# Optimization experiments

Measured on AMD Instinct MI355X. Metric: run time of the kernel, lower is better.

## Reference

```python
import jax, jax.numpy as jnp
import numpy as np

# Module hyperparameters (match torch init_kwargs)
D_MODEL = 512
N_HEADS = 8
WINDOW_LEN = 128
DIL_FACTOR = 64
N_DIL = 2
ATTN_SINK = True
SRC_LEN = 2048
BSZ = 2


def setup_inputs() -> dict:
    key = jax.random.key(0)
    ks = jax.random.split(key, 6)
    w_scale = 0.04  # ~ xavier_uniform scale for 512x512
    inp = {
        "x": jax.random.normal(ks[0], (SRC_LEN, BSZ, D_MODEL), jnp.float32),
        "Wq": jax.random.normal(ks[1], (D_MODEL, D_MODEL), jnp.float32) * w_scale,
        "bq": jnp.zeros((D_MODEL,), jnp.float32),
        "Wk": jax.random.normal(ks[2], (D_MODEL, D_MODEL), jnp.float32) * w_scale,
        "bk": jnp.zeros((D_MODEL,), jnp.float32),
        "Wv": jax.random.normal(ks[3], (D_MODEL, D_MODEL), jnp.float32) * w_scale,
        "bv": jnp.zeros((D_MODEL,), jnp.float32),
        "Wo": jax.random.normal(ks[4], (D_MODEL, D_MODEL), jnp.float32) * w_scale,
        "bo": jnp.zeros((D_MODEL,), jnp.float32),
        "beta": jnp.zeros((N_HEADS,), jnp.float32),
    }
    return inp


def _fast_attention(x, Wq, bq, Wk, bk, Wv, bv, Wo, bo, beta):
    s, b, dm = x.shape  # (src_len, bsz, d_model)
    h = N_HEADS
    d = dm // h
    q = x @ Wq.T + bq
    k = x @ Wk.T + bk
    v = x @ Wv.T + bv

    def split_heads(t):  # 's b (h d) -> (b h) s d'
        return t.reshape(s, b, h, d).transpose(1, 2, 0, 3).reshape(b * h, s, d)

    q, k, v = split_heads(q), split_heads(k), split_heads(v)

    # beta: per-head temperature, tiled over batch (matches torch .repeat(bsz,1,1))
    beta_e = jnp.tile(jnp.exp(beta), b)[:, None, None]  # (b*h, 1, 1)
    q = q / (jnp.sqrt(jnp.asarray(d, q.dtype)) * beta_e)

    attn_out = jnp.zeros_like(v)
    z = b * h
    for i in range(N_DIL):
        dil = DIL_FACTOR ** i
        p = (WINDOW_LEN - 1) * dil
        pad = (p % s) if (p % s) != p else 0  # static python ints
        nw = pad // dil + 1  # num windows
        # causal left-padded strided windowed view of q: (z, nw, s, d)
        qp = jnp.pad(q, ((0, 0), (pad, 0), (0, 0)))
        idx = (jnp.arange(nw) * dil)[:, None] + jnp.arange(s)[None, :]  # (nw, s)
        qi = qp[:, idx, :]
        w = jnp.einsum('zbsd,zsd->zbs', qi, k)  # (z, nw, s)
        if ATTN_SINK:
            w = jnp.concatenate([w, jnp.zeros((z, 1, s), w.dtype)], axis=1)
        w = jax.nn.softmax(w, axis=1)  # softmax over window axis (+ sink)
        if ATTN_SINK:
            w = w[:, :-1]
        k2 = jnp.einsum('zbs,zsd->zbd', w, k)  # (z, nw, d)
        v2 = jnp.einsum('zbs,zsd->zbd', w, v)
        # left-pad back to full length (zeros at front, values at end)
        k = jnp.pad(k2, ((0, 0), (s - nw, 0), (0, 0)))
        v = jnp.pad(v2, ((0, 0), (s - nw, 0), (0, 0)))
        attn_out = attn_out + v

    # '(b h) s d -> s b (h d)'
    out = attn_out.reshape(b, h, s, d).transpose(2, 0, 1, 3).reshape(s, b, dm)
    return out @ Wo.T + bo


def reference(x, Wq, bq, Wk, bk, Wv, bv, Wo, bo, beta):
    return _fast_attention(x, Wq, bq, Wk, bk, Wv, bv, Wo, bo, beta)
```

## Files before the change

### kernel.cpp

```cpp
#include <hip/hip_runtime.h>
#include <hip/hip_bf16.h>
#include <math.h>

#define S_LEN 2048
#define BSZ 2
#define DM 512
#define NH 8
#define HD 64
#define RTOT (S_LEN*BSZ)
#define T_KEEP 32
#define ROW0 ((S_LEN - T_KEEP)*BSZ)
#define NXELEM (RTOT*DM)
#define NWROW  (NH*128)
#define NWELEM (NWROW*DM)

typedef __attribute__((ext_vector_type(8))) _Float16 half8;
typedef __attribute__((ext_vector_type(4))) float floatx4;

__device__ __forceinline__ void gld16(const void* g, void* l) {
    __builtin_amdgcn_global_load_lds((const __attribute__((address_space(1))) void*)g,
                                     (__attribute__((address_space(3))) void*)l, 16, 0, 0);
}

__device__ __forceinline__ short cvt1(float v) {
    _Float16 h = (_Float16)v;
    return __builtin_bit_cast(short, h);
}

__global__ __launch_bounds__(256) void convert(
    const float* __restrict__ x,
    const float* __restrict__ Wq, const float* __restrict__ Wk,
    const float* __restrict__ bq, const float* __restrict__ bk,
    const float* __restrict__ bo,
    short* __restrict__ xf, short* __restrict__ wf, float* __restrict__ bcat,
    float* __restrict__ sig, float* __restrict__ sbar, float* __restrict__ Ssum,
    float* __restrict__ out)
{
    const int g = blockIdx.x*blockDim.x + threadIdx.x;
    const int stride = gridDim.x*blockDim.x;
    const int total4 = (NXELEM + NWELEM)/4;
    for (int i = g; i < total4; i += stride) {
        float4 v; size_t dst; short* d;
        if (i < NXELEM/4) {
            v = ((const float4*)x)[i];
            dst = (size_t)i*4; d = xf;
        } else {
            int e = (i - NXELEM/4)*4;
            int R = e >> 9;
            int k = e & 511;
            int h = R >> 7;
            int p = R & 127;
            int m = p >> 6;
            int c = p & 63;
            const float* W = m ? Wk : Wq;
            v = *(const float4*)&W[(size_t)(h*HD + c)*DM + k];
            dst = (size_t)R*DM + k; d = wf;
        }
        short4 hv;
        hv.x = cvt1(v.x); hv.y = cvt1(v.y); hv.z = cvt1(v.z); hv.w = cvt1(v.w);
        *(short4*)&d[dst] = hv;
    }
    {
        const float4* b4 = (const float4*)bo;
        float4* o4 = (float4*)out;
        const int fill4 = ROW0*DM/4;
        for (int i = g; i < fill4; i += stride) o4[i] = b4[i & 127];
    }
    if (g < NWROW) {
        int h = g >> 7, p = g & 127, m = p >> 6, c = p & 63;
        bcat[g] = (m ? bk : bq)[h*HD + c];
    }
    if (g < NH*RTOT) sig[g] = 0.f;
    if (g < 16*DM)   sbar[g] = 0.f;
    if (g < 16)      Ssum[g] = 0.f;
}

__global__ __launch_bounds__(256, 2) void qk_gemm(
    const _Float16* __restrict__ xf, const _Float16* __restrict__ wf,
    const float* __restrict__ bcat,
    float* __restrict__ sig, float* __restrict__ qsel)
{
    __shared__ __align__(16) char smem[65536];

    const int tid  = threadIdx.x;
    const int w    = tid >> 6;
    const int lane = tid & 63;
    const int lrow = lane & 15;
    const int lk8  = lane >> 4;
    const int rc   = blockIdx.x;
    const int h    = blockIdx.y;
    const int jh   = blockIdx.z;
    const int r0   = rc * 128;

    {
        const int t = w;
        const int bcol = (t < 2) ? (jh*32 + t*16) : (64 + jh*32 + (t-2)*16);
        const _Float16* src = wf + (size_t)(h*128 + bcol + lrow)*DM + lk8*8;
        for (int ci = 0; ci < 16; ++ci)
            gld16(src + ci*32, smem + (w*16 + ci)*1024);
    }
    __syncthreads();

    const float bq0 = bcat[h*128 + jh*32 + lrow];
    const float bq1 = bcat[h*128 + jh*32 + 16 + lrow];
    const float bk0 = bcat[h*128 + 64 + jh*32 + lrow];
    const float bk1 = bcat[h*128 + 64 + jh*32 + 16 + lrow];

    #pragma unroll
    for (int nn = 0; nn < 2; ++nn) {
        const int n = w + nn*4;
        const int rbase = r0 + n*16;

        half8 A[16];
        const _Float16* pa = xf + (size_t)(rbase + lrow)*DM + lk8*8;
        #pragma unroll
        for (int kc = 0; kc < 16; ++kc)
            A[kc] = *(const half8*)(pa + kc*32);

        floatx4 aq0 = (floatx4)0.f, aq1 = (floatx4)0.f;
        floatx4 ak0 = (floatx4)0.f, ak1 = (floatx4)0.f;
        #pragma unroll
        for (int kc = 0; kc < 16; ++kc) {
            half8 b0 = *(const half8*)(smem + ( 0 + kc)*1024 + lane*16);
            half8 b1 = *(const half8*)(smem + (16 + kc)*1024 + lane*16);
            half8 b2 = *(const half8*)(smem + (32 + kc)*1024 + lane*16);
            half8 b3 = *(const half8*)(smem + (48 + kc)*1024 + lane*16);
            aq0 = __builtin_amdgcn_mfma_f32_16x16x32_f16(A[kc], b0, aq0, 0, 0, 0);
            aq1 = __builtin_amdgcn_mfma_f32_16x16x32_f16(A[kc], b1, aq1, 0, 0, 0);
            ak0 = __builtin_amdgcn_mfma_f32_16x16x32_f16(A[kc], b2, ak0, 0, 0, 0);
            ak1 = __builtin_amdgcn_mfma_f32_16x16x32_f16(A[kc], b3, ak1, 0, 0, 0);
        }

        #pragma unroll
        for (int r = 0; r < 4; ++r) {
            float q0 = aq0[r] + bq0, q1 = aq1[r] + bq1;
            float k0 = ak0[r] + bk0, k1 = ak1[r] + bk1;
            float p = q0*k0 + q1*k1;
            p += __shfl_xor(p, 1, 64);
            p += __shfl_xor(p, 2, 64);
            p += __shfl_xor(p, 4, 64);
            p += __shfl_xor(p, 8, 64);
            int row = rbase + lk8*4 + r;
            if (lrow == 0) atomicAdd(&sig[h*RTOT + row], p);
            if (((row >> 1) & 63) == 63) {
                int b  = row & 1;
                int wi = row >> 7;
                float* qd = &qsel[((size_t)(b*NH + h)*T_KEEP + wi)*64];
                qd[jh*32 + lrow]      = q0;
                qd[jh*32 + 16 + lrow] = q1;
            }
        }
    }
}

__global__ __launch_bounds__(256) void sbark(
    const float* __restrict__ x, const float* __restrict__ sigr,
    const float* __restrict__ beta, float* __restrict__ sbar,
    float* __restrict__ Ssum)
{
    __shared__ float ss[64][NH];
    const int tid = threadIdx.x;
    const int b = blockIdx.x & 1;
    const int s0 = (blockIdx.x >> 1) * 64;

    for (int i = tid; i < 64*NH; i += 256) {
        int s = i >> 3, hh = i & 7;
        float raw = sigr[hh*RTOT + (s0 + s)*2 + b];
        float isc = 1.0f / (8.0f * expf(beta[hh]));
        ss[s][hh] = 1.0f / (1.0f + expf(-raw * isc));
    }
    __syncthreads();
    if (tid < NH) {
        float t = 0.f;
        for (int s = 0; s < 64; ++s) t += ss[s][tid];
        atomicAdd(&Ssum[b*NH + tid], t);
    }
    #pragma unroll
    for (int cp = 0; cp < 2; ++cp) {
        int c = cp*256 + tid;
        float a8[NH];
        #pragma unroll
        for (int hh = 0; hh < NH; ++hh) a8[hh] = 0.f;
        for (int s = 0; s < 64; ++s) {
            float xv = x[(size_t)((s0 + s)*2 + b)*DM + c];
            #pragma unroll
            for (int hh = 0; hh < NH; ++hh) a8[hh] += ss[s][hh] * xv;
        }
        #pragma unroll
        for (int hh = 0; hh < NH; ++hh)
            atomicAdd(&sbar[(b*NH + hh)*DM + c], a8[hh]);
    }
}

__global__ __launch_bounds__(256) void headk(
    const float* __restrict__ qsel, const float* __restrict__ beta,
    const float* __restrict__ sbar, const float* __restrict__ Ssum,
    const float* __restrict__ Wk, const float* __restrict__ bk,
    const float* __restrict__ Wv, const float* __restrict__ bv,
    const float* __restrict__ Wo,
    float* __restrict__ coef, float* __restrict__ G)
{
    const int z = blockIdx.x;
    const int h = z & 7;
    const int tid = threadIdx.x;

    __shared__ float s_sb[DM];
    __shared__ float s_red[64][4];
    __shared__ float s_kb[64], s_vb[64];
    __shared__ float s_part[T_KEEP][8];
    __shared__ float s_gp[64][4];

    s_sb[tid]       = sbar[z*DM + tid];
    s_sb[tid + 256] = sbar[z*DM + 256 + tid];
    __syncthreads();
    const float S = Ssum[z];

    {
        int j = tid >> 2, kp = tid & 3;
        const float* wr = &Wk[(size_t)(h*HD + j)*DM + kp*128];
        float a = 0.f;
        #pragma unroll
        for (int k = 0; k < 128; k += 4) {
            float4 w4 = *(const float4*)&wr[k];
            int k0 = kp*128 + k;
            a += w4.x*s_sb[k0] + w4.y*s_sb[k0+1] + w4.z*s_sb[k0+2] + w4.w*s_sb[k0+3];
        }
        s_red[j][kp] = a;
    }
    __syncthreads();
    if (tid < 64) s_kb[tid] = s_red[tid][0]+s_red[tid][1]+s_red[tid][2]+s_red[tid][3]
                              + bk[h*HD + tid]*S;
    __syncthreads();
    {
        int j = tid >> 2, kp = tid & 3;
        const float* wr = &Wv[(size_t)(h*HD + j)*DM + kp*128];
        float a = 0.f;
        #pragma unroll
        for (int k = 0; k < 128; k += 4) {
            float4 w4 = *(const float4*)&wr[k];
            int k0 = kp*128 + k;
            a += w4.x*s_sb[k0] + w4.y*s_sb[k0+1] + w4.z*s_sb[k0+2] + w4.w*s_sb[k0+3];
        }
        s_red[j][kp] = a;
    }
    __syncthreads();
    if (tid < 64) s_vb[tid] = s_red[tid][0]+s_red[tid][1]+s_red[tid][2]+s_red[tid][3]
                              + bv[h*HD + tid]*S;
    __syncthreads();

    {
        int wi = tid >> 3, jg = tid & 7;
        const float* qrow = &qsel[((size_t)z*T_KEEP + wi)*64 + jg*8];
        float4 q1 = *(const float4*)qrow;
        float4 q2 = *(const float4*)(qrow + 4);
        int j0 = jg*8;
        float p = q1.x*s_kb[j0] + q1.y*s_kb[j0+1] + q1.z*s_kb[j0+2] + q1.w*s_kb[j0+3]
                + q2.x*s_kb[j0+4] + q2.y*s_kb[j0+5] + q2.z*s_kb[j0+6] + q2.w*s_kb[j0+7];
        s_part[wi][jg] = p;
    }
    __syncthreads();
    if (tid < T_KEEP) {
        float sc = 0.f;
        #pragma unroll
        for (int gg = 0; gg < 8; ++gg) sc += s_part[tid][gg];
        sc *= 1.0f / (8.0f * expf(beta[h]));
        float m = sc;
        #pragma unroll
        for (int off = 16; off > 0; off >>= 1) m = fmaxf(m, __shfl_xor(m, off, 64));
        m = fmaxf(m, 0.f);
        float e = expf(sc - m);
        float d = e;
        #pragma unroll
        for (int off = 16; off > 0; off >>= 1) d += __shfl_xor(d, off, 64);
        d += expf(-m);
        float c = e / d;
        if (tid == T_KEEP-1) c += 1.0f;
        coef[z*T_KEEP + tid] = c;
    }

    const int cq = tid >> 2;
    const int jg = tid & 3;
    #pragma unroll
    for (int it = 0; it < 8; ++it) {
        int c = it*64 + cq;
        const float* wrow = &Wo[(size_t)c*DM + h*HD + jg*16];
        float a = 0.f;
        #pragma unroll
        for (int jj = 0; jj < 16; jj += 4) {
            float4 wv = *(const float4*)&wrow[jj];
            int j0 = jg*16 + jj;
            a += wv.x*s_vb[j0] + wv.y*s_vb[j0+1] + wv.z*s_vb[j0+2] + wv.w*s_vb[j0+3];
        }
        s_gp[cq][jg] = a;
        __syncthreads();
        if (tid < 64)
            G[(size_t)z*DM + it*64 + tid] = s_gp[tid][0] + s_gp[tid][1] + s_gp[tid][2] + s_gp[tid][3];
        __syncthreads();
    }
}

__global__ __launch_bounds__(256) void outk3(
    const float* __restrict__ coef, const float* __restrict__ G,
    const float* __restrict__ bo, float* __restrict__ out)
{
    const int a = blockIdx.x;
    const int b = a & 1;
    const int wi = a >> 1;
    const int tid = threadIdx.x;
    __shared__ float s_cf[NH];
    if (tid < NH) s_cf[tid] = coef[(b*NH + tid)*T_KEEP + wi];
    __syncthreads();
    for (int c = tid; c < DM; c += 256) {
        float v = bo[c];
        #pragma unroll
        for (int h = 0; h < NH; ++h)
            v += s_cf[h] * G[(size_t)(b*NH + h)*DM + c];
        out[(size_t)(ROW0 + a)*DM + c] = v;
    }
}

extern "C" void kernel_launch(void* const* d_in, const int* in_sizes, int n_in,
                              void* d_out, int out_size, void* d_ws, size_t ws_size,
                              hipStream_t stream) {
    const float* x    = (const float*)d_in[0];
    const float* Wq   = (const float*)d_in[1];
    const float* bq   = (const float*)d_in[2];
    const float* Wk   = (const float*)d_in[3];
    const float* bk   = (const float*)d_in[4];
    const float* Wv   = (const float*)d_in[5];
    const float* bv   = (const float*)d_in[6];
    const float* Wo   = (const float*)d_in[7];
    const float* bo   = (const float*)d_in[8];
    const float* beta = (const float*)d_in[9];

    char* ws = (char*)d_ws;
    float* sig  = (float*)(ws + 0);
    float* qsel = (float*)(ws + 131072);
    float* sbar = (float*)(ws + 262144);
    float* Ssum = (float*)(ws + 294912);
    float* bcat = (float*)(ws + 295168);
    float* coef = (float*)(ws + 299264);
    float* G    = (float*)(ws + 301312);
    short* xf   = (short*)(ws + 335872);
    short* wf   = (short*)(ws + 335872 + 4194304);
    float* out  = (float*)d_out;

    convert<<<2048, 256, 0, stream>>>(x, Wq, Wk, bq, bk, bo,
                                      xf, wf, bcat, sig, sbar, Ssum, out);
    dim3 g1(32, NH, 2);
    qk_gemm<<<g1, 256, 0, stream>>>((const _Float16*)xf, (const _Float16*)wf,
                                    bcat, sig, qsel);
    sbark<<<64, 256, 0, stream>>>(x, sig, beta, sbar, Ssum);
    headk<<<16, 256, 0, stream>>>(qsel, beta, sbar, Ssum, Wk, bk, Wv, bv, Wo, coef, G);
    outk3<<<64, 256, 0, stream>>>(coef, G, bo, out);
}
```

Measured before the change: 125.6 us.

## Pre-swizzle fp16 operands into MFMA fragment layout and remove atomics

```diff
diff --git a/kernel.cpp b/kernel.cpp
--- a/kernel.cpp
+++ b/kernel.cpp
@@ -1,5 +1,4 @@
 #include <hip/hip_runtime.h>
-#include <hip/hip_bf16.h>
 #include <math.h>
 
 #define S_LEN 2048
@@ -10,9 +9,6 @@
 #define RTOT (S_LEN*BSZ)
 #define T_KEEP 32
 #define ROW0 ((S_LEN - T_KEEP)*BSZ)
-#define NXELEM (RTOT*DM)
-#define NWROW  (NH*128)
-#define NWELEM (NWROW*DM)
 
 typedef __attribute__((ext_vector_type(8))) _Float16 half8;
 typedef __attribute__((ext_vector_type(4))) float floatx4;
@@ -27,57 +23,57 @@
     return __builtin_bit_cast(short, h);
 }
 
-__global__ __launch_bounds__(256) void convert(
-    const float* __restrict__ x,
-    const float* __restrict__ Wq, const float* __restrict__ Wk,
-    const float* __restrict__ bq, const float* __restrict__ bk,
-    const float* __restrict__ bo,
-    short* __restrict__ xf, short* __restrict__ wf, float* __restrict__ bcat,
-    float* __restrict__ sig, float* __restrict__ sbar, float* __restrict__ Ssum,
-    float* __restrict__ out)
-{
-    const int g = blockIdx.x*blockDim.x + threadIdx.x;
-    const int stride = gridDim.x*blockDim.x;
-    const int total4 = (NXELEM + NWELEM)/4;
-    for (int i = g; i < total4; i += stride) {
-        float4 v; size_t dst; short* d;
-        if (i < NXELEM/4) {
-            v = ((const float4*)x)[i];
-            dst = (size_t)i*4; d = xf;
-        } else {
-            int e = (i - NXELEM/4)*4;
-            int R = e >> 9;
-            int k = e & 511;
-            int h = R >> 7;
-            int p = R & 127;
-            int m = p >> 6;
-            int c = p & 63;
-            const float* W = m ? Wk : Wq;
-            v = *(const float4*)&W[(size_t)(h*HD + c)*DM + k];
-            dst = (size_t)R*DM + k; d = wf;
-        }
-        short4 hv;
-        hv.x = cvt1(v.x); hv.y = cvt1(v.y); hv.z = cvt1(v.z); hv.w = cvt1(v.w);
-        *(short4*)&d[dst] = hv;
-    }
-    {
+__global__ __launch_bounds__(256) void convert2(
+    const float* __restrict__ x, const float* __restrict__ Wq,
+    const float* __restrict__ Wk, const float* __restrict__ bo,
+    short* __restrict__ xfrag, short* __restrict__ wfrag, float* __restrict__ out)
+{
+    __shared__ short sm[8192];
+    const int bx = blockIdx.x;
+    const int tid = threadIdx.x;
+    if (bx >= 320) {
+        int g = (bx - 320)*256 + tid;
         const float4* b4 = (const float4*)bo;
         float4* o4 = (float4*)out;
         const int fill4 = ROW0*DM/4;
-        for (int i = g; i < fill4; i += stride) o4[i] = b4[i & 127];
-    }
-    if (g < NWROW) {
-        int h = g >> 7, p = g & 127, m = p >> 6, c = p & 63;
-        bcat[g] = (m ? bk : bq)[h*HD + c];
-    }
-    if (g < NH*RTOT) sig[g] = 0.f;
-    if (g < 16*DM)   sbar[g] = 0.f;
-    if (g < 16)      Ssum[g] = 0.f;
+        for (int i = g; i < fill4; i += 512*256) o4[i] = b4[i & 127];
+        return;
+    }
+    const float* src;
+    short* dst;
+    if (bx < 256) {
+        src = x + (size_t)bx*16*DM;
+        dst = xfrag + (size_t)bx*16*DM;
+    } else {
+        int wt = bx - 256;
+        int h = wt >> 3, jh = (wt >> 2) & 1, t = wt & 3;
+        int m = t >> 1, sub = t & 1;
+        const float* W = m ? Wk : Wq;
+        src = W + (size_t)(h*HD + jh*32 + sub*16)*DM;
+        dst = wfrag + (size_t)((h*2 + jh)*64 + t*16)*512;
+    }
+    #pragma unroll
+    for (int it = 0; it < 8; ++it) {
+        int f4 = it*256 + tid;
+        int row = f4 >> 7, k4 = f4 & 127;
+        float4 v = ((const float4*)src)[row*128 + k4];
+        short4 hv;
+        hv.x = cvt1(v.x); hv.y = cvt1(v.y); hv.z = cvt1(v.z); hv.w = cvt1(v.w);
+        int kc = k4 >> 3, lk8 = (k4 >> 1) & 3, ho = (k4 & 1)*4;
+        *(short4*)&sm[(kc*64 + lk8*16 + row)*8 + ho] = hv;
+    }
+    __syncthreads();
+    #pragma unroll
+    for (int it = 0; it < 4; ++it) {
+        int p = it*256 + tid;
+        uint4 v = *(const uint4*)&sm[p*8];
+        *(uint4*)&dst[p*8] = v;
+    }
 }
 
 __global__ __launch_bounds__(256, 2) void qk_gemm(
-    const _Float16* __restrict__ xf, const _Float16* __restrict__ wf,
-    const float* __restrict__ bcat,
+    const short* __restrict__ xfrag, const short* __restrict__ wfrag,
+    const float* __restrict__ bq, const float* __restrict__ bk,
     float* __restrict__ sig, float* __restrict__ qsel)
 {
     __shared__ __align__(16) char smem[65536];
@@ -90,32 +86,29 @@
     const int rc   = blockIdx.x;
     const int h    = blockIdx.y;
     const int jh   = blockIdx.z;
-    const int r0   = rc * 128;
-
-    {
-        const int t = w;
-        const int bcol = (t < 2) ? (jh*32 + t*16) : (64 + jh*32 + (t-2)*16);
-        const _Float16* src = wf + (size_t)(h*128 + bcol + lrow)*DM + lk8*8;
+
+    {
+        const short* src = wfrag + ((size_t)(h*2 + jh)*64 + w*16)*512 + lane*8;
         for (int ci = 0; ci < 16; ++ci)
-            gld16(src + ci*32, smem + (w*16 + ci)*1024);
-    }
-    __syncthreads();
-
-    const float bq0 = bcat[h*128 + jh*32 + lrow];
-    const float bq1 = bcat[h*128 + jh*32 + 16 + lrow];
-    const float bk0 = bcat[h*128 + 64 + jh*32 + lrow];
-    const float bk1 = bcat[h*128 + 64 + jh*32 + 16 + lrow];
+            gld16(src + ci*512, smem + (w*16 + ci)*1024);
+    }
+    __syncthreads();
+
+    const float bq0 = bq[h*HD + jh*32 + lrow];
+    const float bq1 = bq[h*HD + jh*32 + 16 + lrow];
+    const float bk0 = bk[h*HD + jh*32 + lrow];
+    const float bk1 = bk[h*HD + jh*32 + 16 + lrow];
 
     #pragma unroll
     for (int nn = 0; nn < 2; ++nn) {
-        const int n = w + nn*4;
-        const int rbase = r0 + n*16;
+        const int rt = rc*8 + w + nn*4;
+        const int rbase = rt*16;
 
         half8 A[16];
-        const _Float16* pa = xf + (size_t)(rbase + lrow)*DM + lk8*8;
+        const short* pa = xfrag + (size_t)rt*8192 + lane*8;
         #pragma unroll
         for (int kc = 0; kc < 16; ++kc)
-            A[kc] = *(const half8*)(pa + kc*32);
+            A[kc] = *(const half8*)(pa + kc*512);
 
         floatx4 aq0 = (floatx4)0.f, aq1 = (floatx4)0.f;
         floatx4 ak0 = (floatx4)0.f, ak1 = (floatx4)0.f;
@@ -141,7 +134,7 @@
             p += __shfl_xor(p, 4, 64);
             p += __shfl_xor(p, 8, 64);
             int row = rbase + lk8*4 + r;
-            if (lrow == 0) atomicAdd(&sig[h*RTOT + row], p);
+            if (lrow == 0) sig[((size_t)jh*NH + h)*RTOT + row] = p;
             if (((row >> 1) & 63) == 63) {
                 int b  = row & 1;
                 int wi = row >> 7;
@@ -154,41 +147,64 @@
 }
 
 __global__ __launch_bounds__(256) void sbark(
-    const float* __restrict__ x, const float* __restrict__ sigr,
+    const float* __restrict__ x, const float* __restrict__ sig,
     const float* __restrict__ beta, float* __restrict__ sbar,
     float* __restrict__ Ssum)
 {
-    __shared__ float ss[64][NH];
+    __shared__ float ss[256*8];
+    __shared__ float s_red[2048];
     const int tid = threadIdx.x;
     const int b = blockIdx.x & 1;
-    const int s0 = (blockIdx.x >> 1) * 64;
-
-    for (int i = tid; i < 64*NH; i += 256) {
-        int s = i >> 3, hh = i & 7;
-        float raw = sigr[hh*RTOT + (s0 + s)*2 + b];
-        float isc = 1.0f / (8.0f * expf(beta[hh]));
-        ss[s][hh] = 1.0f / (1.0f + expf(-raw * isc));
-    }
-    __syncthreads();
-    if (tid < NH) {
-        float t = 0.f;
-        for (int s = 0; s < 64; ++s) t += ss[s][tid];
-        atomicAdd(&Ssum[b*NH + tid], t);
-    }
-    #pragma unroll
-    for (int cp = 0; cp < 2; ++cp) {
-        int c = cp*256 + tid;
-        float a8[NH];
-        #pragma unroll
-        for (int hh = 0; hh < NH; ++hh) a8[hh] = 0.f;
-        for (int s = 0; s < 64; ++s) {
-            float xv = x[(size_t)((s0 + s)*2 + b)*DM + c];
+    const int cc = (blockIdx.x >> 1)*32;
+    const int col = tid & 31, sgrp = tid >> 5;
+    const int hld = tid & 7, sld = tid >> 3;
+    const float is = 1.0f / (8.0f * expf(beta[hld]));
+
+    float a8[8];
+    #pragma unroll
+    for (int hh = 0; hh < 8; ++hh) a8[hh] = 0.f;
+    float tsum = 0.f;
+
+    for (int scn = 0; scn < 8; ++scn) {
+        const int s0 = scn*256;
+        #pragma unroll
+        for (int j = 0; j < 8; ++j) {
+            int sl = sld + 32*j;
+            int s = s0 + sl;
+            float raw = sig[(size_t)hld*RTOT + s*2 + b]
+                      + sig[(size_t)(NH + hld)*RTOT + s*2 + b];
+            float sv = 1.0f / (1.0f + expf(-raw * is));
+            ss[sl*8 + hld] = sv;
+            tsum += sv;
+        }
+        __syncthreads();
+        for (int j = 0; j < 32; ++j) {
+            int sl = sgrp + j*8;
+            float xv = x[(size_t)((s0 + sl)*2 + b)*DM + cc + col];
             #pragma unroll
-            for (int hh = 0; hh < NH; ++hh) a8[hh] += ss[s][hh] * xv;
-        }
-        #pragma unroll
-        for (int hh = 0; hh < NH; ++hh)
-            atomicAdd(&sbar[(b*NH + hh)*DM + c], a8[hh]);
+            for (int hh = 0; hh < 8; ++hh) a8[hh] += ss[sl*8 + hh] * xv;
+        }
+        __syncthreads();
+    }
+    #pragma unroll
+    for (int hh = 0; hh < 8; ++hh) s_red[(sgrp*32 + col)*8 + hh] = a8[hh];
+    __syncthreads();
+    {
+        int hh = tid >> 5, c2 = tid & 31;
+        float a = 0.f;
+        #pragma unroll
+        for (int sg = 0; sg < 8; ++sg) a += s_red[(sg*32 + c2)*8 + hh];
+        sbar[(size_t)(b*NH + hh)*DM + cc + c2] = a;
+    }
+    if (cc == 0) {
+        __syncthreads();
+        s_red[tid] = tsum;
+        __syncthreads();
+        if (tid < 8) {
+            float t = 0.f;
+            for (int i = tid; i < 256; i += 8) t += s_red[i];
+            Ssum[b*NH + tid] = t;
+        }
     }
 }
 
@@ -334,23 +350,20 @@
     const float* beta = (const float*)d_in[9];
 
     char* ws = (char*)d_ws;
-    float* sig  = (float*)(ws + 0);
-    float* qsel = (float*)(ws + 131072);
-    float* sbar = (float*)(ws + 262144);
-    float* Ssum = (float*)(ws + 294912);
-    float* bcat = (float*)(ws + 295168);
-    float* coef = (float*)(ws + 299264);
-    float* G    = (float*)(ws + 301312);
-    short* xf   = (short*)(ws + 335872);
-    short* wf   = (short*)(ws + 335872 + 4194304);
-    float* out  = (float*)d_out;
-
-    convert<<<2048, 256, 0, stream>>>(x, Wq, Wk, bq, bk, bo,
-                                      xf, wf, bcat, sig, sbar, Ssum, out);
+    float* sig   = (float*)(ws + 0);
+    float* qsel  = (float*)(ws + 262144);
+    float* sbar  = (float*)(ws + 393216);
+    float* Ssum  = (float*)(ws + 425984);
+    float* coef  = (float*)(ws + 426240);
+    float* G     = (float*)(ws + 428288);
+    short* xfrag = (short*)(ws + 461056);
+    short* wfrag = (short*)(ws + 461056 + 4194304);
+    float* out   = (float*)d_out;
+
+    convert2<<<832, 256, 0, stream>>>(x, Wq, Wk, bo, xfrag, wfrag, out);
     dim3 g1(32, NH, 2);
-    qk_gemm<<<g1, 256, 0, stream>>>((const _Float16*)xf, (const _Float16*)wf,
-                                    bcat, sig, qsel);
-    sbark<<<64, 256, 0, stream>>>(x, sig, beta, sbar, Ssum);
+    qk_gemm<<<g1, 256, 0, stream>>>(xfrag, wfrag, bq, bk, sig, qsel);
+    sbark<<<32, 256, 0, stream>>>(x, sig, beta, sbar, Ssum);
     headk<<<16, 256, 0, stream>>>(qsel, beta, sbar, Ssum, Wk, bk, Wv, bv, Wo, coef, G);
     outk3<<<64, 256, 0, stream>>>(coef, G, bo, out);
 }
```

Result: slower. 142.2 us (+13.2%).

## Fuse five kernels into one persistent kernel with grid barriers

Applied to the files above, without the earlier changes.

```diff
diff --git a/kernel.cpp b/kernel.cpp
--- a/kernel.cpp
+++ b/kernel.cpp
@@ -1,5 +1,4 @@
 #include <hip/hip_runtime.h>
-#include <hip/hip_bf16.h>
 #include <math.h>
 
 #define S_LEN 2048
@@ -13,6 +12,8 @@
 #define NXELEM (RTOT*DM)
 #define NWROW  (NH*128)
 #define NWELEM (NWROW*DM)
+#define GRID   512
+#define NTHR   (GRID*256)
 
 typedef __attribute__((ext_vector_type(8))) _Float16 half8;
 typedef __attribute__((ext_vector_type(4))) float floatx4;
@@ -27,295 +28,301 @@
     return __builtin_bit_cast(short, h);
 }
 
-__global__ __launch_bounds__(256) void convert(
+__device__ __forceinline__ void gridbar(unsigned* cnt, int idx) {
+    __syncthreads();
+    __threadfence();
+    if (threadIdx.x == 0) {
+        atomicAdd(&cnt[idx], 1u);
+        unsigned it = 0;
+        while (atomicAdd(&cnt[idx], 0u) < (unsigned)GRID && it < 2000000u) {
+            __builtin_amdgcn_s_sleep(8);
+            ++it;
+        }
+    }
+    __syncthreads();
+    __threadfence();
+}
+
+__global__ __launch_bounds__(256, 2) void fused(
     const float* __restrict__ x,
-    const float* __restrict__ Wq, const float* __restrict__ Wk,
-    const float* __restrict__ bq, const float* __restrict__ bk,
-    const float* __restrict__ bo,
+    const float* __restrict__ Wq, const float* __restrict__ bq,
+    const float* __restrict__ Wk, const float* __restrict__ bk,
+    const float* __restrict__ Wv, const float* __restrict__ bv,
+    const float* __restrict__ Wo, const float* __restrict__ bo,
+    const float* __restrict__ beta,
     short* __restrict__ xf, short* __restrict__ wf, float* __restrict__ bcat,
-    float* __restrict__ sig, float* __restrict__ sbar, float* __restrict__ Ssum,
-    float* __restrict__ out)
-{
-    const int g = blockIdx.x*blockDim.x + threadIdx.x;
-    const int stride = gridDim.x*blockDim.x;
-    const int total4 = (NXELEM + NWELEM)/4;
-    for (int i = g; i < total4; i += stride) {
-        float4 v; size_t dst; short* d;
-        if (i < NXELEM/4) {
-            v = ((const float4*)x)[i];
-            dst = (size_t)i*4; d = xf;
-        } else {
-            int e = (i - NXELEM/4)*4;
-            int R = e >> 9;
-            int k = e & 511;
-            int h = R >> 7;
-            int p = R & 127;
-            int m = p >> 6;
-            int c = p & 63;
-            const float* W = m ? Wk : Wq;
-            v = *(const float4*)&W[(size_t)(h*HD + c)*DM + k];
-            dst = (size_t)R*DM + k; d = wf;
-        }
-        short4 hv;
-        hv.x = cvt1(v.x); hv.y = cvt1(v.y); hv.z = cvt1(v.z); hv.w = cvt1(v.w);
-        *(short4*)&d[dst] = hv;
-    }
-    {
-        const float4* b4 = (const float4*)bo;
-        float4* o4 = (float4*)out;
-        const int fill4 = ROW0*DM/4;
-        for (int i = g; i < fill4; i += stride) o4[i] = b4[i & 127];
-    }
-    if (g < NWROW) {
-        int h = g >> 7, p = g & 127, m = p >> 6, c = p & 63;
-        bcat[g] = (m ? bk : bq)[h*HD + c];
-    }
-    if (g < NH*RTOT) sig[g] = 0.f;
-    if (g < 16*DM)   sbar[g] = 0.f;
-    if (g < 16)      Ssum[g] = 0.f;
-}
-
-__global__ __launch_bounds__(256, 2) void qk_gemm(
-    const _Float16* __restrict__ xf, const _Float16* __restrict__ wf,
-    const float* __restrict__ bcat,
-    float* __restrict__ sig, float* __restrict__ qsel)
+    float* __restrict__ sig, float* __restrict__ qsel,
+    float* __restrict__ sbar, float* __restrict__ Ssum,
+    float* __restrict__ coef, float* __restrict__ G,
+    unsigned* __restrict__ cnt, float* __restrict__ out)
 {
     __shared__ __align__(16) char smem[65536];
-
-    const int tid  = threadIdx.x;
-    const int w    = tid >> 6;
-    const int lane = tid & 63;
-    const int lrow = lane & 15;
-    const int lk8  = lane >> 4;
-    const int rc   = blockIdx.x;
-    const int h    = blockIdx.y;
-    const int jh   = blockIdx.z;
-    const int r0   = rc * 128;
+    const int bid = blockIdx.x;
+    const int tid = threadIdx.x;
 
     {
-        const int t = w;
-        const int bcol = (t < 2) ? (jh*32 + t*16) : (64 + jh*32 + (t-2)*16);
-        const _Float16* src = wf + (size_t)(h*128 + bcol + lrow)*DM + lk8*8;
-        for (int ci = 0; ci < 16; ++ci)
-            gld16(src + ci*32, smem + (w*16 + ci)*1024);
-    }
-    __syncthreads();
-
-    const float bq0 = bcat[h*128 + jh*32 + lrow];
-    const float bq1 = bcat[h*128 + jh*32 + 16 + lrow];
-    const float bk0 = bcat[h*128 + 64 + jh*32 + lrow];
-    const float bk1 = bcat[h*128 + 64 + jh*32 + 16 + lrow];
-
-    #pragma unroll
-    for (int nn = 0; nn < 2; ++nn) {
-        const int n = w + nn*4;
-        const int rbase = r0 + n*16;
-
-        half8 A[16];
-        const _Float16* pa = xf + (size_t)(rbase + lrow)*DM + lk8*8;
+        const int g = bid*256 + tid;
+        const int total4 = (NXELEM + NWELEM)/4;
+        for (int i = g; i < total4; i += NTHR) {
+            float4 v; size_t dst; short* d;
+            if (i < NXELEM/4) {
+                v = ((const float4*)x)[i];
+                dst = (size_t)i*4; d = xf;
+            } else {
+                int e = (i - NXELEM/4)*4;
+                int R = e >> 9;
+                int k = e & 511;
+                int h = R >> 7;
+                int p = R & 127;
+                int m = p >> 6;
+                int c = p & 63;
+                const float* W = m ? Wk : Wq;
+                v = *(const float4*)&W[(size_t)(h*HD + c)*DM + k];
+                dst = (size_t)R*DM + k; d = wf;
+            }
+            short4 hv;
+            hv.x = cvt1(v.x); hv.y = cvt1(v.y); hv.z = cvt1(v.z); hv.w = cvt1(v.w);
+            *(short4*)&d[dst] = hv;
+        }
+        {
+            const float4* b4 = (const float4*)bo;
+            float4* o4 = (float4*)out;
+            const int fill4 = ROW0*DM/4;
+            for (int i = g; i < fill4; i += NTHR) o4[i] = b4[i & 127];
+        }
+        if (g < NWROW) {
+            int h = g >> 7, p = g & 127, m = p >> 6, c = p & 63;
+            bcat[g] = (m ? bk : bq)[h*HD + c];
+        }
+        if (g < NH*RTOT) sig[g] = 0.f;
+        if (g < 16*DM)   sbar[g] = 0.f;
+        if (g < 16)      Ssum[g] = 0.f;
+    }
+    gridbar(cnt, 0);
+
+    {
+        const int w    = tid >> 6;
+        const int lane = tid & 63;
+        const int lrow = lane & 15;
+        const int lk8  = lane >> 4;
+        const int rc   = bid & 31;
+        const int h    = (bid >> 5) & 7;
+        const int jh   = bid >> 8;
+        const int r0   = rc * 128;
+
+        {
+            const int t = w;
+            const int bcol = (t < 2) ? (jh*32 + t*16) : (64 + jh*32 + (t-2)*16);
+            const short* src = wf + (size_t)(h*128 + bcol + lrow)*DM + lk8*8;
+            for (int ci = 0; ci < 16; ++ci)
+                gld16(src + ci*32, smem + (w*16 + ci)*1024);
+        }
+        __syncthreads();
+
+        const float bq0 = bcat[h*128 + jh*32 + lrow];
+        const float bq1 = bcat[h*128 + jh*32 + 16 + lrow];
+        const float bk0 = bcat[h*128 + 64 + jh*32 + lrow];
+        const float bk1 = bcat[h*128 + 64 + jh*32 + 16 + lrow];
+
         #pragma unroll
-        for (int kc = 0; kc < 16; ++kc)
-            A[kc] = *(const half8*)(pa + kc*32);
-
-        floatx4 aq0 = (floatx4)0.f, aq1 = (floatx4)0.f;
-        floatx4 ak0 = (floatx4)0.f, ak1 = (floatx4)0.f;
+        for (int nn = 0; nn < 2; ++nn) {
+            const int n = w + nn*4;
+            const int rbase = r0 + n*16;
+
+            half8 A[16];
+            const short* pa = xf + (size_t)(rbase + lrow)*DM + lk8*8;
+            #pragma unroll
+            for (int kc = 0; kc < 16; ++kc)
+                A[kc] = *(const half8*)(pa + kc*32);
+
+            floatx4 aq0 = (floatx4)0.f, aq1 = (floatx4)0.f;
+            floatx4 ak0 = (floatx4)0.f, ak1 = (floatx4)0.f;
+            #pragma unroll
+            for (int kc = 0; kc < 16; ++kc) {
+                half8 b0 = *(const half8*)(smem + ( 0 + kc)*1024 + lane*16);
+                half8 b1 = *(const half8*)(smem + (16 + kc)*1024 + lane*16);
+                half8 b2 = *(const half8*)(smem + (32 + kc)*1024 + lane*16);
+                half8 b3 = *(const half8*)(smem + (48 + kc)*1024 + lane*16);
+                aq0 = __builtin_amdgcn_mfma_f32_16x16x32_f16(A[kc], b0, aq0, 0, 0, 0);
+                aq1 = __builtin_amdgcn_mfma_f32_16x16x32_f16(A[kc], b1, aq1, 0, 0, 0);
+                ak0 = __builtin_amdgcn_mfma_f32_16x16x32_f16(A[kc], b2, ak0, 0, 0, 0);
+                ak1 = __builtin_amdgcn_mfma_f32_16x16x32_f16(A[kc], b3, ak1, 0, 0, 0);
+            }
+
+            #pragma unroll
+            for (int r = 0; r < 4; ++r) {
+                float q0 = aq0[r] + bq0, q1 = aq1[r] + bq1;
+                float k0 = ak0[r] + bk0, k1 = ak1[r] + bk1;
+                float p = q0*k0 + q1*k1;
+                p += __shfl_xor(p, 1, 64);
+                p += __shfl_xor(p, 2, 64);
+                p += __shfl_xor(p, 4, 64);
+                p += __shfl_xor(p, 8, 64);
+                int row = rbase + lk8*4 + r;
+                if (lrow == 0) atomicAdd(&sig[h*RTOT + row], p);
+                if (((row >> 1) & 63) == 63) {
+                    int b  = row & 1;
+                    int wi = row >> 7;
+                    float* qd = &qsel[((size_t)(b*NH + h)*T_KEEP + wi)*64];
+                    qd[jh*32 + lrow]      = q0;
+                    qd[jh*32 + 16 + lrow] = q1;
+                }
+            }
+        }
+    }
+    gridbar(cnt, 1);
+
+    if (bid < 64) {
+        float* ss = (float*)smem;
+        const int b = bid & 1;
+        const int s0 = (bid >> 1) * 64;
+
+        for (int i = tid; i < 64*NH; i += 256) {
+            int s = i >> 3, hh = i & 7;
+            float raw = sig[hh*RTOT + (s0 + s)*2 + b];
+            float isc = 1.0f / (8.0f * expf(beta[hh]));
+            ss[s*8 + hh] = 1.0f / (1.0f + expf(-raw * isc));
+        }
+        __syncthreads();
+        if (tid < NH) {
+            float t = 0.f;
+            for (int s = 0; s < 64; ++s) t += ss[s*8 + tid];
+            atomicAdd(&Ssum[b*NH + tid], t);
+        }
         #pragma unroll
-        for (int kc = 0; kc < 16; ++kc) {
-            half8 b0 = *(const half8*)(smem + ( 0 + kc)*1024 + lane*16);
-            half8 b1 = *(const half8*)(smem + (16 + kc)*1024 + lane*16);
-            half8 b2 = *(const half8*)(smem + (32 + kc)*1024 + lane*16);
-            half8 b3 = *(const half8*)(smem + (48 + kc)*1024 + lane*16);
-            aq0 = __builtin_amdgcn_mfma_f32_16x16x32_f16(A[kc], b0, aq0, 0, 0, 0);
-            aq1 = __builtin_amdgcn_mfma_f32_16x16x32_f16(A[kc], b1, aq1, 0, 0, 0);
-            ak0 = __builtin_amdgcn_mfma_f32_16x16x32_f16(A[kc], b2, ak0, 0, 0, 0);
-            ak1 = __builtin_amdgcn_mfma_f32_16x16x32_f16(A[kc], b3, ak1, 0, 0, 0);
-        }
-
+        for (int cp = 0; cp < 2; ++cp) {
+            int c = cp*256 + tid;
+            float a8[NH];
+            #pragma unroll
+            for (int hh = 0; hh < NH; ++hh) a8[hh] = 0.f;
+            for (int s = 0; s < 64; ++s) {
+                float xv = x[(size_t)((s0 + s)*2 + b)*DM + c];
+                #pragma unroll
+                for (int hh = 0; hh < NH; ++hh) a8[hh] += ss[s*8 + hh] * xv;
+            }
+            #pragma unroll
+            for (int hh = 0; hh < NH; ++hh)
+                atomicAdd(&sbar[(b*NH + hh)*DM + c], a8[hh]);
+        }
+    }
+    gridbar(cnt, 2);
+
+    if (bid < 16) {
+        float* F = (float*)smem;
+        float* s_sb   = F;
+        float* s_red  = F + 512;
+        float* s_kb   = F + 768;
+        float* s_vb   = F + 832;
+        float* s_part = F + 896;
+        float* s_gp   = F + 1152;
+        const int z = bid;
+        const int h = z & 7;
+
+        s_sb[tid]       = sbar[z*DM + tid];
+        s_sb[tid + 256] = sbar[z*DM + 256 + tid];
+        __syncthreads();
+        const float S = Ssum[z];
+
+        {
+            int j = tid >> 2, kp = tid & 3;
+            const float* wr = &Wk[(size_t)(h*HD + j)*DM + kp*128];
+            float a = 0.f;
+            #pragma unroll
+            for (int k = 0; k < 128; k += 4) {
+                float4 w4 = *(const float4*)&wr[k];
+                int k0 = kp*128 + k;
+                a += w4.x*s_sb[k0] + w4.y*s_sb[k0+1] + w4.z*s_sb[k0+2] + w4.w*s_sb[k0+3];
+            }
+            s_red[j*4 + kp] = a;
+        }
+        __syncthreads();
+        if (tid < 64) s_kb[tid] = s_red[tid*4]+s_red[tid*4+1]+s_red[tid*4+2]+s_red[tid*4+3]
+                                  + bk[h*HD + tid]*S;
+        __syncthreads();
+        {
+            int j = tid >> 2, kp = tid & 3;
+            const float* wr = &Wv[(size_t)(h*HD + j)*DM + kp*128];
+            float a = 0.f;
+            #pragma unroll
+            for (int k = 0; k < 128; k += 4) {
+                float4 w4 = *(const float4*)&wr[k];
+                int k0 = kp*128 + k;
+                a += w4.x*s_sb[k0] + w4.y*s_sb[k0+1] + w4.z*s_sb[k0+2] + w4.w*s_sb[k0+3];
+            }
+            s_red[j*4 + kp] = a;
+        }
+        __syncthreads();
+        if (tid < 64) s_vb[tid] = s_red[tid*4]+s_red[tid*4+1]+s_red[tid*4+2]+s_red[tid*4+3]
+                                  + bv[h*HD + tid]*S;
+        __syncthreads();
+
+        {
+            int wi = tid >> 3, jg = tid & 7;
+            const float* qrow = &qsel[((size_t)z*T_KEEP + wi)*64 + jg*8];
+            float4 q1 = *(const float4*)qrow;
+            float4 q2 = *(const float4*)(qrow + 4);
+            int j0 = jg*8;
+            float p = q1.x*s_kb[j0] + q1.y*s_kb[j0+1] + q1.z*s_kb[j0+2] + q1.w*s_kb[j0+3]
+                    + q2.x*s_kb[j0+4] + q2.y*s_kb[j0+5] + q2.z*s_kb[j0+6] + q2.w*s_kb[j0+7];
+            s_part[wi*8 + jg] = p;
+        }
+        __syncthreads();
+        if (tid < T_KEEP) {
+            float sc = 0.f;
+            #pragma unroll
+            for (int gg = 0; gg < 8; ++gg) sc += s_part[tid*8 + gg];
+            sc *= 1.0f / (8.0f * expf(beta[h]));
+            float m = sc;
+            #pragma unroll
+            for (int off = 16; off > 0; off >>= 1) m = fmaxf(m, __shfl_xor(m, off, 64));
+            m = fmaxf(m, 0.f);
+            float e = expf(sc - m);
+            float d = e;
+            #pragma unroll
+            for (int off = 16; off > 0; off >>= 1) d += __shfl_xor(d, off, 64);
+            d += expf(-m);
+            float c = e / d;
+            if (tid == T_KEEP-1) c += 1.0f;
+            coef[z*T_KEEP + tid] = c;
+        }
+
+        const int cq = tid >> 2;
+        const int jg = tid & 3;
         #pragma unroll
-        for (int r = 0; r < 4; ++r) {
-            float q0 = aq0[r] + bq0, q1 = aq1[r] + bq1;
-            float k0 = ak0[r] + bk0, k1 = ak1[r] + bk1;
-            float p = q0*k0 + q1*k1;
-            p += __shfl_xor(p, 1, 64);
-            p += __shfl_xor(p, 2, 64);
-            p += __shfl_xor(p, 4, 64);
-            p += __shfl_xor(p, 8, 64);
-            int row = rbase + lk8*4 + r;
-            if (lrow == 0) atomicAdd(&sig[h*RTOT + row], p);
-            if (((row >> 1) & 63) == 63) {
-                int b  = row & 1;
-                int wi = row >> 7;
-                float* qd = &qsel[((size_t)(b*NH + h)*T_KEEP + wi)*64];
-                qd[jh*32 + lrow]      = q0;
-                qd[jh*32 + 16 + lrow] = q1;
-            }
-        }
-    }
-}
-
-__global__ __launch_bounds__(256) void sbark(
-    const float* __restrict__ x, const float* __restrict__ sigr,
-    const float* __restrict__ beta, float* __restrict__ sbar,
-    float* __restrict__ Ssum)
-{
-    __shared__ float ss[64][NH];
-    const int tid = threadIdx.x;
-    const int b = blockIdx.x & 1;
-    const int s0 = (blockIdx.x >> 1) * 64;
-
-    for (int i = tid; i < 64*NH; i += 256) {
-        int s = i >> 3, hh = i & 7;
-        float raw = sigr[hh*RTOT + (s0 + s)*2 + b];
-        float isc = 1.0f / (8.0f * expf(beta[hh]));
-        ss[s][hh] = 1.0f / (1.0f + expf(-raw * isc));
-    }
-    __syncthreads();
-    if (tid < NH) {
-        float t = 0.f;
-        for (int s = 0; s < 64; ++s) t += ss[s][tid];
-        atomicAdd(&Ssum[b*NH + tid], t);
-    }
-    #pragma unroll
-    for (int cp = 0; cp < 2; ++cp) {
-        int c = cp*256 + tid;
-        float a8[NH];
-        #pragma unroll
-        for (int hh = 0; hh < NH; ++hh) a8[hh] = 0.f;
-        for (int s = 0; s < 64; ++s) {
-            float xv = x[(size_t)((s0 + s)*2 + b)*DM + c];
-            #pragma unroll
-            for (int hh = 0; hh < NH; ++hh) a8[hh] += ss[s][hh] * xv;
-        }
-        #pragma unroll
-        for (int hh = 0; hh < NH; ++hh)
-            atomicAdd(&sbar[(b*NH + hh)*DM + c], a8[hh]);
-    }
-}
-
-__global__ __launch_bounds__(256) void headk(
-    const float* __restrict__ qsel, const float* __restrict__ beta,
-    const float* __restrict__ sbar, const float* __restrict__ Ssum,
-    const float* __restrict__ Wk, const float* __restrict__ bk,
-    const float* __restrict__ Wv, const float* __restrict__ bv,
-    const float* __restrict__ Wo,
-    float* __restrict__ coef, float* __restrict__ G)
-{
-    const int z = blockIdx.x;
-    const int h = z & 7;
-    const int tid = threadIdx.x;
-
-    __shared__ float s_sb[DM];
-    __shared__ float s_red[64][4];
-    __shared__ float s_kb[64], s_vb[64];
-    __shared__ float s_part[T_KEEP][8];
-    __shared__ float s_gp[64][4];
-
-    s_sb[tid]       = sbar[z*DM + tid];
-    s_sb[tid + 256] = sbar[z*DM + 256 + tid];
-    __syncthreads();
-    const float S = Ssum[z];
-
-    {
-        int j = tid >> 2, kp = tid & 3;
-        const float* wr = &Wk[(size_t)(h*HD + j)*DM + kp*128];
-        float a = 0.f;
-        #pragma unroll
-        for (int k = 0; k < 128; k += 4) {
-            float4 w4 = *(const float4*)&wr[k];
-            int k0 = kp*128 + k;
-            a += w4.x*s_sb[k0] + w4.y*s_sb[k0+1] + w4.z*s_sb[k0+2] + w4.w*s_sb[k0+3];
-        }
-        s_red[j][kp] = a;
-    }
-    __syncthreads();
-    if (tid < 64) s_kb[tid] = s_red[tid][0]+s_red[tid][1]+s_red[tid][2]+s_red[tid][3]
-                              + bk[h*HD + tid]*S;
-    __syncthreads();
-    {
-        int j = tid >> 2, kp = tid & 3;
-        const float* wr = &Wv[(size_t)(h*HD + j)*DM + kp*128];
-        float a = 0.f;
-        #pragma unroll
-        for (int k = 0; k < 128; k += 4) {
-            float4 w4 = *(const float4*)&wr[k];
-            int k0 = kp*128 + k;
-            a += w4.x*s_sb[k0] + w4.y*s_sb[k0+1] + w4.z*s_sb[k0+2] + w4.w*s_sb[k0+3];
-        }
-        s_red[j][kp] = a;
-    }
-    __syncthreads();
-    if (tid < 64) s_vb[tid] = s_red[tid][0]+s_red[tid][1]+s_red[tid][2]+s_red[tid][3]
-                              + bv[h*HD + tid]*S;
-    __syncthreads();
-
-    {
-        int wi = tid >> 3, jg = tid & 7;
-        const float* qrow = &qsel[((size_t)z*T_KEEP + wi)*64 + jg*8];
-        float4 q1 = *(const float4*)qrow;
-        float4 q2 = *(const float4*)(qrow + 4);
-        int j0 = jg*8;
-        float p = q1.x*s_kb[j0] + q1.y*s_kb[j0+1] + q1.z*s_kb[j0+2] + q1.w*s_kb[j0+3]
-                + q2.x*s_kb[j0+4] + q2.y*s_kb[j0+5] + q2.z*s_kb[j0+6] + q2.w*s_kb[j0+7];
-        s_part[wi][jg] = p;
-    }
-    __syncthreads();
-    if (tid < T_KEEP) {
-        float sc = 0.f;
-        #pragma unroll
-        for (int gg = 0; gg < 8; ++gg) sc += s_part[tid][gg];
-        sc *= 1.0f / (8.0f * expf(beta[h]));
-        float m = sc;
-        #pragma unroll
-        for (int off = 16; off > 0; off >>= 1) m = fmaxf(m, __shfl_xor(m, off, 64));
-        m = fmaxf(m, 0.f);
-        float e = expf(sc - m);
-        float d = e;
-        #pragma unroll
-        for (int off = 16; off > 0; off >>= 1) d += __shfl_xor(d, off, 64);
-        d += expf(-m);
-        float c = e / d;
-        if (tid == T_KEEP-1) c += 1.0f;
-        coef[z*T_KEEP + tid] = c;
-    }
-
-    const int cq = tid >> 2;
-    const int jg = tid & 3;
-    #pragma unroll
-    for (int it = 0; it < 8; ++it) {
-        int c = it*64 + cq;
-        const float* wrow = &Wo[(size_t)c*DM + h*HD + jg*16];
-        float a = 0.f;
-        #pragma unroll
-        for (int jj = 0; jj < 16; jj += 4) {
-            float4 wv = *(const float4*)&wrow[jj];
-            int j0 = jg*16 + jj;
-            a += wv.x*s_vb[j0] + wv.y*s_vb[j0+1] + wv.z*s_vb[j0+2] + wv.w*s_vb[j0+3];
-        }
-        s_gp[cq][jg] = a;
-        __syncthreads();
-        if (tid < 64)
-            G[(size_t)z*DM + it*64 + tid] = s_gp[tid][0] + s_gp[tid][1] + s_gp[tid][2] + s_gp[tid][3];
-        __syncthreads();
-    }
-}
-
-__global__ __launch_bounds__(256) void outk3(
-    const float* __restrict__ coef, const float* __restrict__ G,
-    const float* __restrict__ bo, float* __restrict__ out)
-{
-    const int a = blockIdx.x;
-    const int b = a & 1;
-    const int wi = a >> 1;
-    const int tid = threadIdx.x;
-    __shared__ float s_cf[NH];
-    if (tid < NH) s_cf[tid] = coef[(b*NH + tid)*T_KEEP + wi];
-    __syncthreads();
-    for (int c = tid; c < DM; c += 256) {
-        float v = bo[c];
-        #pragma unroll
-        for (int h = 0; h < NH; ++h)
-            v += s_cf[h] * G[(size_t)(b*NH + h)*DM + c];
-        out[(size_t)(ROW0 + a)*DM + c] = v;
+        for (int it = 0; it < 8; ++it) {
+            int c = it*64 + cq;
+            const float* wrow = &Wo[(size_t)c*DM + h*HD + jg*16];
+            float a = 0.f;
+            #pragma unroll
+            for (int jj = 0; jj < 16; jj += 4) {
+                float4 wv = *(const float4*)&wrow[jj];
+                int j0 = jg*16 + jj;
+                a += wv.x*s_vb[j0] + wv.y*s_vb[j0+1] + wv.z*s_vb[j0+2] + wv.w*s_vb[j0+3];
+            }
+            s_gp[cq*4 + jg] = a;
+            __syncthreads();
+            if (tid < 64)
+                G[(size_t)z*DM + it*64 + tid] = s_gp[tid*4] + s_gp[tid*4+1] + s_gp[tid*4+2] + s_gp[tid*4+3];
+            __syncthreads();
+        }
+    }
+    gridbar(cnt, 3);
+
+    if (bid < 64) {
+        float* s_cf = (float*)smem;
+        const int a = bid;
+        const int b = a & 1;
+        const int wi = a >> 1;
+        __syncthreads();
+        if (tid < NH) s_cf[tid] = coef[(b*NH + tid)*T_KEEP + wi];
+        __syncthreads();
+        for (int c = tid; c < DM; c += 256) {
+            float v = bo[c];
+            #pragma unroll
+            for (int h = 0; h < NH; ++h)
+                v += s_cf[h] * G[(size_t)(b*NH + h)*DM + c];
+            out[(size_t)(ROW0 + a)*DM + c] = v;
+        }
     }
 }
 
@@ -343,14 +350,11 @@
     float* G    = (float*)(ws + 301312);
     short* xf   = (short*)(ws + 335872);
     short* wf   = (short*)(ws + 335872 + 4194304);
+    unsigned* cnt = (unsigned*)(ws + 335872 + 4194304 + 1048576);
     float* out  = (float*)d_out;
 
-    convert<<<2048, 256, 0, stream>>>(x, Wq, Wk, bq, bk, bo,
-                                      xf, wf, bcat, sig, sbar, Ssum, out);
-    dim3 g1(32, NH, 2);
-    qk_gemm<<<g1, 256, 0, stream>>>((const _Float16*)xf, (const _Float16*)wf,
-                                    bcat, sig, qsel);
-    sbark<<<64, 256, 0, stream>>>(x, sig, beta, sbar, Ssum);
-    headk<<<16, 256, 0, stream>>>(qsel, beta, sbar, Ssum, Wk, bk, Wv, bv, Wo, coef, G);
-    outk3<<<64, 256, 0, stream>>>(coef, G, bo, out);
-}
+    hipMemsetAsync(cnt, 0, 4*sizeof(unsigned), stream);
+    fused<<<GRID, 256, 0, stream>>>(x, Wq, bq, Wk, bk, Wv, bv, Wo, bo, beta,
+                                    xf, wf, bcat, sig, qsel, sbar, Ssum,
+                                    coef, G, cnt, out);
+}
```

After: 455.8 us. +262.8%, slower.
